# Optimization experiments

Hardware: AMD Instinct MI355X
Metric: run time of the kernel (lower is better)

Reference implementation:

```python
import jax, jax.numpy as jnp
import numpy as np

N, E, F_IN, HID, OUT, H = 50000, 500000, 128, 64, 64, 2
P_DROP = 0.2


def setup_inputs() -> dict:
    key = jax.random.key(0)
    ks = jax.random.split(key, 24)
    g = lambda k, shp: jax.random.normal(k, shp, jnp.float32) * 0.05
    inp = {
        "feat": jax.random.normal(ks[0], (N, F_IN), jnp.float32),
        "edge_src": jax.random.randint(ks[1], (E,), 0, N, jnp.int32),
        "edge_dst": jax.random.randint(ks[2], (E,), 0, N, jnp.int32),
        # feature-mask linears
        "Wmt": g(ks[3], (F_IN, F_IN)), "bmt": g(ks[4], (F_IN,)),
        "Wms": g(ks[5], (F_IN, F_IN)), "bms": g(ks[6], (F_IN,)),
        # SAGEConv layers (mean aggregator): self + neigh linear + bias
        "W1_self": g(ks[7], (F_IN, HID)), "W1_neigh": g(ks[8], (F_IN, HID)), "b1": g(ks[9], (HID,)),
        "W2_self": g(ks[10], (HID, OUT)), "W2_neigh": g(ks[11], (HID, OUT)), "b2": g(ks[12], (OUT,)),
        # GATv2Conv layers: fc_src, fc_dst, attn vector per head, bias
        "g1_Wsrc": g(ks[13], (F_IN, H * HID)), "g1_Wdst": g(ks[14], (F_IN, H * HID)),
        "g1_attn": g(ks[15], (H, HID)), "g1_bias": g(ks[16], (H * HID,)),
        "g2_Wsrc": g(ks[17], (HID, H * OUT)), "g2_Wdst": g(ks[18], (HID, H * OUT)),
        "g2_attn": g(ks[19], (H, OUT)), "g2_bias": g(ks[20], (H * OUT,)),
        # final projection
        "W3": g(ks[21], (OUT + F_IN, OUT)), "b3": g(ks[22], (OUT,)),
    }
    # deterministic (inverted) dropout masks, training=True, p=0.2
    keep = 1.0 - P_DROP
    km1, km2 = jax.random.split(ks[23])
    inp["drop_t"] = jax.random.bernoulli(km1, keep, (N, HID)).astype(jnp.float32) / keep
    inp["drop_s"] = jax.random.bernoulli(km2, keep, (N, HID)).astype(jnp.float32) / keep
    return inp


def _sage_mean(h, src, dst, W_self, W_neigh, b):
    # mean over in-neighbors, then linear (mean and linear commute)
    agg = jax.ops.segment_sum(h[src], dst, num_segments=N)          # [N,D]
    deg = jax.ops.segment_sum(jnp.ones((E,), h.dtype), dst, num_segments=N)
    h_neigh = agg / jnp.maximum(deg, 1.0)[:, None]
    return h @ W_self + h_neigh @ W_neigh + b


def _gatv2(h, src, dst, Wsrc, Wdst, attn, bias, heads, dout):
    fs = (h @ Wsrc).reshape(N, heads, dout)
    fd = (h @ Wdst).reshape(N, heads, dout)
    e = jax.nn.leaky_relu(fs[src] + fd[dst], 0.2)                   # [E,H,D]
    logits = jnp.einsum('ehd,hd->eh', e, attn)                      # [E,H]
    m = jax.ops.segment_max(logits, dst, num_segments=N)            # edge softmax per dst
    ex = jnp.exp(logits - m[dst])
    denom = jax.ops.segment_sum(ex, dst, num_segments=N)
    alpha = ex / denom[dst]                                         # [E,H]
    out = jax.ops.segment_sum(alpha[:, :, None] * fs[src], dst, num_segments=N)
    return out + bias.reshape(heads, dout)                          # [N,H,D]


def _l2norm(x):
    return x / jnp.maximum(jnp.linalg.norm(x, axis=1, keepdims=True), 1e-12)


def reference(feat, edge_src, edge_dst, Wmt, bmt, Wms, bms,
              W1_self, W1_neigh, b1, W2_self, W2_neigh, b2,
              g1_Wsrc, g1_Wdst, g1_attn, g1_bias,
              g2_Wsrc, g2_Wdst, g2_attn, g2_bias,
              W3, b3, drop_t, drop_s):
    gelu = lambda x: jax.nn.gelu(x, approximate=False)  # torch F.gelu default = exact erf
    # topology branch (SAGE)
    h_t = feat * jax.nn.sigmoid(feat @ Wmt + bmt)
    h_t = gelu(_sage_mean(h_t, edge_src, edge_dst, W1_self, W1_neigh, b1)) * drop_t
    h_t = gelu(_sage_mean(h_t, edge_src, edge_dst, W2_self, W2_neigh, b2))
    h_t = jnp.concatenate([h_t, feat], axis=1) @ W3 + b3
    h_t = _l2norm(jax.nn.leaky_relu(h_t, 0.01))
    # semantic branch (GATv2)
    h_s = feat * jax.nn.sigmoid(feat @ Wms + bms)
    h_s = gelu(_gatv2(h_s, edge_src, edge_dst, g1_Wsrc, g1_Wdst, g1_attn, g1_bias, H, HID)).mean(axis=1) * drop_s
    h_s = gelu(_gatv2(h_s, edge_src, edge_dst, g2_Wsrc, g2_Wdst, g2_attn, g2_bias, H, OUT)).mean(axis=1)
    h_s = _l2norm(h_s)
    return (h_t, h_s)
```

## Files before the change

kernel.cpp:

```cpp
#include <hip/hip_runtime.h>
#include <math.h>

constexpr int N_  = 50000;
constexpr int E_  = 500000;
constexpr int NB_ = (N_ + 255) / 256;

typedef unsigned short u16;
typedef unsigned int u32;
typedef short short8 __attribute__((ext_vector_type(8)));
typedef __bf16 bf16x8 __attribute__((ext_vector_type(8)));
typedef float f32x4 __attribute__((ext_vector_type(4)));
typedef short short4v __attribute__((ext_vector_type(4)));

#define DINL __device__ __forceinline__

DINL float gelu_f(float x) { return 0.5f * x * (1.f + erff(x * 0.70710678118654752f)); }
DINL float sigmoid_f(float x) { return 1.f / (1.f + expf(-x)); }
DINL u16 f2b(float x) {
  unsigned u = __float_as_uint(x);
  return (u16)((u + 0x7FFFu + ((u >> 16) & 1u)) >> 16);
}
DINL float b2f(u16 b) { return __uint_as_float(((unsigned)b) << 16); }

template <int CTRL>
DINL float dpp_add(float c) {
  int p = __builtin_amdgcn_update_dpp(0, __builtin_bit_cast(int, c), CTRL, 0xf, 0xf, false);
  return c + __builtin_bit_cast(float, p);
}
DINL float reduce16(float c) {
  c = dpp_add<0xB1>(c);
  c = dpp_add<0x4E>(c);
  c = dpp_add<0x141>(c);
  c = dpp_add<0x140>(c);
  return c;
}

__global__ void deg_int_kernel(const int* __restrict__ dst, int* __restrict__ deg) {
  int t = blockIdx.x * 256 + threadIdx.x;
  if (t < E_) atomicAdd(&deg[dst[t]], 1);
}

__global__ __launch_bounds__(256) void scan_local(const int* __restrict__ deg,
    int* __restrict__ rowptr, int* __restrict__ bsum) {
  __shared__ int sums[4];
  const int tid = threadIdx.x, lane = tid & 63, wid = tid >> 6;
  const int i = blockIdx.x * 256 + tid;
  int v = (i < N_) ? deg[i] : 0;
  int x = v;
#pragma unroll
  for (int o = 1; o < 64; o <<= 1) { int y = __shfl_up(x, o); if (lane >= o) x += y; }
  if (lane == 63) sums[wid] = x;
  __syncthreads();
  int woff = 0;
#pragma unroll
  for (int w = 0; w < 3; ++w) if (w < wid) woff += sums[w];
  if (i < N_) rowptr[i] = x - v + woff;
  if (tid == 255) bsum[blockIdx.x] = woff + x;
}

__global__ __launch_bounds__(256) void scan_block(const int* __restrict__ bsum,
                                                  int* __restrict__ bpre) {
  __shared__ int sums[4];
  const int tid = threadIdx.x, lane = tid & 63, wid = tid >> 6;
  int v = (tid < NB_) ? bsum[tid] : 0;
  int x = v;
#pragma unroll
  for (int o = 1; o < 64; o <<= 1) { int y = __shfl_up(x, o); if (lane >= o) x += y; }
  if (lane == 63) sums[wid] = x;
  __syncthreads();
  int woff = 0;
#pragma unroll
  for (int w = 0; w < 3; ++w) if (w < wid) woff += sums[w];
  if (tid < NB_) bpre[tid] = x - v + woff;
  if (tid == 255) bpre[NB_] = woff + x;
}

__global__ __launch_bounds__(256) void scan_add(int* __restrict__ rowptr,
                                                const int* __restrict__ bpre) {
  int i = blockIdx.x * 256 + threadIdx.x;
  if (i < N_) rowptr[i] += bpre[i >> 8];
  else if (i == N_) rowptr[N_] = bpre[NB_];
}

__global__ void csr_fill(const int* __restrict__ src, const int* __restrict__ dst,
                         const int* __restrict__ rowptr, int* __restrict__ cursor,
                         int* __restrict__ colsrc) {
  int e = blockIdx.x * 256 + threadIdx.x;
  if (e >= E_) return;
  int d = dst[e];
  int pos = rowptr[d] + atomicAdd(&cursor[d], 1);
  colsrc[pos] = src[e];
}

__global__ __launch_bounds__(256) void pack_feat(const float* __restrict__ f,
                                                 u16* __restrict__ o) {
  int t = blockIdx.x * 256 + threadIdx.x;
  float4 v = ((const float4*)f)[t];
  short4v r;
  r[0] = (short)f2b(v.x); r[1] = (short)f2b(v.y);
  r[2] = (short)f2b(v.z); r[3] = (short)f2b(v.w);
  ((short4v*)o)[t] = r;
}

__global__ __launch_bounds__(256) void pack_w(
    const float* __restrict__ Wmt, const float* __restrict__ Wms,
    const float* __restrict__ W1s, const float* __restrict__ W1n,
    const float* __restrict__ W2s, const float* __restrict__ W2n,
    const float* __restrict__ g1Ws, const float* __restrict__ g1Wd,
    const float* __restrict__ g2Ws, const float* __restrict__ g2Wd,
    const float* __restrict__ W3, u16* __restrict__ dst) {
  int e = blockIdx.x * 256 + threadIdx.x;
  const float *Wa, *Wb = nullptr;
  int K1, K2 = 0, Ca, Cb = 0, st;
  if (e < 16384)       { Wa = Wmt;  K1 = 128; Ca = 128;           st = 0; }
  else if (e < 32768)  { Wa = Wms;  K1 = 128; Ca = 128;           st = 16384; }
  else if (e < 49152)  { Wa = W1s;  Wb = W1n; K1 = 128; K2 = 128; Ca = 64;  st = 32768; }
  else if (e < 57344)  { Wa = W2s;  Wb = W2n; K1 = 64;  K2 = 64;  Ca = 64;  st = 49152; }
  else if (e < 90112)  { Wa = g1Ws; Wb = g1Wd; K1 = 128; Ca = 128; Cb = 128; st = 57344; }
  else if (e < 106496) { Wa = g2Ws; Wb = g2Wd; K1 = 64;  Ca = 128; Cb = 128; st = 90112; }
  else                 { Wa = W3;   K1 = 192; Ca = 64;            st = 106496; }
  int el = e - st;
  int Kt = K1 + K2;
  int ct = el / (Kt * 16);
  int rem = el - ct * Kt * 16;
  int ks = rem >> 9, rem2 = rem & 511, lane = rem2 >> 3, j = rem2 & 7;
  int k = ks * 32 + ((lane >> 4) << 3) + j;
  int c = ct * 16 + (lane & 15);
  float v;
  if (k < K1) v = (c < Ca) ? Wa[k * Ca + c] : Wb[k * Cb + (c - Ca)];
  else        v = Wb[(k - K1) * Ca + c];
  dst[e] = f2b(v);
}

template <int K1, int K2, int C, int EPI>
__global__ __launch_bounds__(512) void gemm_mfma(
    const u16* __restrict__ A1, const u16* __restrict__ A2,
    const u16* __restrict__ Wp, const float* __restrict__ bias,
    const float* __restrict__ bias2, const float* __restrict__ mulf,
    void* __restrict__ outv, void* __restrict__ outv2) {
  constexpr int K = K1 + K2, KS = K / 32, CT4 = C / 64;
  constexpr int NCH1 = K1 / 8, NCH2 = K2 / 8;
  __shared__ u16 alds[64 * K];
  const int tid = threadIdx.x;
  const int w = tid >> 6, l = tid & 63;
  const int cq = w >> 1, rh = w & 1;
  const int wr0 = blockIdx.x * 64;

  short8 wfrag[KS][CT4];
#pragma unroll
  for (int ks = 0; ks < KS; ++ks)
#pragma unroll
    for (int c4 = 0; c4 < CT4; ++c4)
      wfrag[ks][c4] = *(const short8*)(Wp +
          ((size_t)((cq * CT4 + c4) * KS + ks) * 64 + l) * 8);

  for (int i = tid; i < 64 * NCH1; i += 512) {
    int rr = i / NCH1, kc = i % NCH1;
    int gr = wr0 + rr; if (gr >= N_) gr = N_ - 1;
    short8 v = *(const short8*)(A1 + (long)gr * K1 + kc * 8);
    *(short8*)&alds[rr * K + ((kc ^ (rr & 7)) << 3)] = v;
  }
  if constexpr (K2 > 0) {
    for (int i = tid; i < 64 * NCH2; i += 512) {
      int rr = i / NCH2, kc = i % NCH2;
      int gr = wr0 + rr; if (gr >= N_) gr = N_ - 1;
      short8 v = *(const short8*)(A2 + (long)gr * K2 + kc * 8);
      *(short8*)&alds[rr * K + (((NCH1 + kc) ^ (rr & 7)) << 3)] = v;
    }
  }
  __syncthreads();

  f32x4 acc[2][CT4];
#pragma unroll
  for (int rr = 0; rr < 2; ++rr)
#pragma unroll
    for (int c4 = 0; c4 < CT4; ++c4) acc[rr][c4] = (f32x4){0.f, 0.f, 0.f, 0.f};

#pragma unroll
  for (int ks = 0; ks < KS; ++ks) {
#pragma unroll
    for (int rr = 0; rr < 2; ++rr) {
      const int nr = (rh * 2 + rr) * 16 + (l & 15);
      const int ch = (ks * 4 + (l >> 4)) ^ (nr & 7);
      short8 av = *(const short8*)&alds[nr * K + (ch << 3)];
      bf16x8 bf = __builtin_bit_cast(bf16x8, av);
#pragma unroll
      for (int c4 = 0; c4 < CT4; ++c4)
        acc[rr][c4] = __builtin_amdgcn_mfma_f32_16x16x32_bf16(
            __builtin_bit_cast(bf16x8, wfrag[ks][c4]), bf, acc[rr][c4], 0, 0, 0);
    }
  }

  const int colq = (l >> 4) << 2;
  if constexpr (EPI == 0) {
    u16* out = (u16*)outv;
#pragma unroll
    for (int rr = 0; rr < 2; ++rr) {
      int row = wr0 + (rh * 2 + rr) * 16 + (l & 15);
      if (row >= N_) continue;
#pragma unroll
      for (int c4 = 0; c4 < CT4; ++c4) {
        int colb = (cq * CT4 + c4) * 16 + colq;
        short4v s;
#pragma unroll
        for (int r = 0; r < 4; ++r) s[r] = (short)f2b(acc[rr][c4][r]);
        *(short4v*)(out + (long)row * C + colb) = s;
      }
    }
  } else if constexpr (EPI == 2 || EPI == 3) {
    u16* out = (u16*)outv;
    const int colb = cq * 16 + colq;
    float4 bv = *(const float4*)(bias + colb);
#pragma unroll
    for (int rr = 0; rr < 2; ++rr) {
      int row = wr0 + (rh * 2 + rr) * 16 + (l & 15);
      if (row >= N_) continue;
      float4 dv;
      if constexpr (EPI == 2) dv = *(const float4*)(mulf + (long)row * C + colb);
      short4v s;
#pragma unroll
      for (int r = 0; r < 4; ++r) {
        float g = gelu_f(acc[rr][0][r] + ((const float*)&bv)[r]);
        if constexpr (EPI == 2) g *= ((const float*)&dv)[r];
        s[r] = (short)f2b(g);
      }
      *(short4v*)(out + (long)row * C + colb) = s;
    }
  } else if constexpr (EPI == 4) {
    __shared__ float ssb[64][4];
    float* out = (float*)outv;
    const int colb = cq * 16 + colq;
    float4 bv = *(const float4*)(bias + colb);
    float xv[2][4];
#pragma unroll
    for (int rr = 0; rr < 2; ++rr) {
      float ss = 0.f;
#pragma unroll
      for (int r = 0; r < 4; ++r) {
        float x = acc[rr][0][r] + ((const float*)&bv)[r];
        x = fmaxf(x, 0.01f * x);
        xv[rr][r] = x; ss += x * x;
      }
      ss += __shfl_xor(ss, 16);
      ss += __shfl_xor(ss, 32);
      if (l < 16) ssb[(rh * 2 + rr) * 16 + l][cq] = ss;
    }
    __syncthreads();
#pragma unroll
    for (int rr = 0; rr < 2; ++rr) {
      int nl = (rh * 2 + rr) * 16 + (l & 15);
      int row = wr0 + nl;
      if (row >= N_) continue;
      float ss = ssb[nl][0] + ssb[nl][1] + ssb[nl][2] + ssb[nl][3];
      float sc = 1.f / fmaxf(sqrtf(ss), 1e-12f);
      float4 o;
#pragma unroll
      for (int r = 0; r < 4; ++r) ((float*)&o)[r] = xv[rr][r] * sc;
      *(float4*)(out + (long)row * 64 + colb) = o;
    }
  } else {
#pragma unroll
    for (int c4 = 0; c4 < CT4; ++c4) {
      const int ct = cq * CT4 + c4;
      const bool lo = ct < 8;
      u16* op = lo ? (u16*)outv : (u16*)outv2;
      const int ccb = (ct & 7) * 16 + colq;
      float4 bv = *(const float4*)((lo ? bias : bias2) + ccb);
#pragma unroll
      for (int rr = 0; rr < 2; ++rr) {
        int nl = (rh * 2 + rr) * 16 + (l & 15);
        int row = wr0 + nl;
        if (row >= N_) continue;
        int ch = (ccb >> 3) ^ (nl & 7);
        short4v fq = *(const short4v*)&alds[nl * K + (ch << 3) + (ccb & 7)];
        short4v s;
#pragma unroll
        for (int r = 0; r < 4; ++r) {
          float x = acc[rr][c4][r] + ((const float*)&bv)[r];
          float fv = b2f((u16)fq[r]);
          s[r] = (short)f2b(fv * sigmoid_f(x));
        }
        *(short4v*)(op + (long)row * 128 + ccb) = s;
      }
    }
  }
}

__global__ __launch_bounds__(256) void gather_bf128(const u16* __restrict__ h,
    const int* __restrict__ rowptr, const int* __restrict__ colsrc,
    u16* __restrict__ out) {
  int node = blockIdx.x * 4 + (threadIdx.x >> 6);
  int l = threadIdx.x & 63;
  int hl = l & 31, half = l >> 5;
  int beg = rowptr[node], end = rowptr[node + 1];
  float inv = 1.f / fmaxf((float)(end - beg), 1.f);
  float a0 = 0.f, a1 = 0.f, a2 = 0.f, a3 = 0.f;
  float b0 = 0.f, b1 = 0.f, b2 = 0.f, b3 = 0.f;
  const int off = 4 * hl;
  int j = beg;
  for (; j + 8 <= end; j += 8) {
    int sa = colsrc[j + half],     sb = colsrc[j + 2 + half];
    int sc = colsrc[j + 4 + half], sd = colsrc[j + 6 + half];
    uint2 va = *(const uint2*)(h + (size_t)sa * 128 + off);
    uint2 vb = *(const uint2*)(h + (size_t)sb * 128 + off);
    uint2 vc = *(const uint2*)(h + (size_t)sc * 128 + off);
    uint2 vd = *(const uint2*)(h + (size_t)sd * 128 + off);
    a0 += b2f((u16)(va.x & 0xffffu)) + b2f((u16)(vc.x & 0xffffu));
    a1 += b2f((u16)(va.x >> 16))     + b2f((u16)(vc.x >> 16));
    a2 += b2f((u16)(va.y & 0xffffu)) + b2f((u16)(vc.y & 0xffffu));
    a3 += b2f((u16)(va.y >> 16))     + b2f((u16)(vc.y >> 16));
    b0 += b2f((u16)(vb.x & 0xffffu)) + b2f((u16)(vd.x & 0xffffu));
    b1 += b2f((u16)(vb.x >> 16))     + b2f((u16)(vd.x >> 16));
    b2 += b2f((u16)(vb.y & 0xffffu)) + b2f((u16)(vd.y & 0xffffu));
    b3 += b2f((u16)(vb.y >> 16))     + b2f((u16)(vd.y >> 16));
  }
  for (; j < end; j += 2) {
    int idx = j + half;
    bool valid = idx < end;
    int s = colsrc[valid ? idx : end - 1];
    uint2 v = *(const uint2*)(h + (size_t)s * 128 + off);
    if (!valid) { v.x = 0; v.y = 0; }
    a0 += b2f((u16)(v.x & 0xffffu));
    a1 += b2f((u16)(v.x >> 16));
    a2 += b2f((u16)(v.y & 0xffffu));
    a3 += b2f((u16)(v.y >> 16));
  }
  a0 += b0; a1 += b1; a2 += b2; a3 += b3;
  a0 += __shfl_xor(a0, 32); a1 += __shfl_xor(a1, 32);
  a2 += __shfl_xor(a2, 32); a3 += __shfl_xor(a3, 32);
  if (l < 32) {
    short4v s;
    s[0] = (short)f2b(a0 * inv); s[1] = (short)f2b(a1 * inv);
    s[2] = (short)f2b(a2 * inv); s[3] = (short)f2b(a3 * inv);
    *(short4v*)(out + (long)node * 128 + off) = s;
  }
}

__global__ __launch_bounds__(256) void gather_bf64(const u16* __restrict__ h,
    const int* __restrict__ rowptr, const int* __restrict__ colsrc,
    u16* __restrict__ out) {
  int node = blockIdx.x * 4 + (threadIdx.x >> 6);
  int l = threadIdx.x & 63;
  int ql = l & 15, qg = l >> 4;
  int beg = rowptr[node], end = rowptr[node + 1];
  float a0 = 0.f, a1 = 0.f, a2 = 0.f, a3 = 0.f;
  float b0 = 0.f, b1 = 0.f, b2 = 0.f, b3 = 0.f;
  const int off = 4 * ql;
  int j = beg;
  for (; j + 8 <= end; j += 8) {
    int s0 = colsrc[j + qg], s1 = colsrc[j + 4 + qg];
    uint2 v0 = *(const uint2*)(h + (size_t)s0 * 64 + off);
    uint2 v1 = *(const uint2*)(h + (size_t)s1 * 64 + off);
    a0 += b2f((u16)(v0.x & 0xffffu));
    a1 += b2f((u16)(v0.x >> 16));
    a2 += b2f((u16)(v0.y & 0xffffu));
    a3 += b2f((u16)(v0.y >> 16));
    b0 += b2f((u16)(v1.x & 0xffffu));
    b1 += b2f((u16)(v1.x >> 16));
    b2 += b2f((u16)(v1.y & 0xffffu));
    b3 += b2f((u16)(v1.y >> 16));
  }
  for (; j < end; j += 4) {
    int idx = j + qg;
    bool valid = idx < end;
    int s = colsrc[valid ? idx : end - 1];
    uint2 v = *(const uint2*)(h + (size_t)s * 64 + off);
    if (!valid) { v.x = 0; v.y = 0; }
    a0 += b2f((u16)(v.x & 0xffffu));
    a1 += b2f((u16)(v.x >> 16));
    a2 += b2f((u16)(v.y & 0xffffu));
    a3 += b2f((u16)(v.y >> 16));
  }
  a0 += b0; a1 += b1; a2 += b2; a3 += b3;
  a0 += __shfl_xor(a0, 32); a1 += __shfl_xor(a1, 32);
  a2 += __shfl_xor(a2, 32); a3 += __shfl_xor(a3, 32);
  a0 += __shfl_xor(a0, 16); a1 += __shfl_xor(a1, 16);
  a2 += __shfl_xor(a2, 16); a3 += __shfl_xor(a3, 16);
  if (l < 16) {
    float inv = 1.f / fmaxf((float)(end - beg), 1.f);
    short4v s;
    s[0] = (short)f2b(a0 * inv); s[1] = (short)f2b(a1 * inv);
    s[2] = (short)f2b(a2 * inv); s[3] = (short)f2b(a3 * inv);
    *(short4v*)(out + (long)node * 64 + off) = s;
  }
}

template <bool LAYER1>
__global__ __launch_bounds__(256) void gat_fused(const u16* __restrict__ fsfd,
    const int* __restrict__ rowptr, const int* __restrict__ colsrc,
    const float* __restrict__ attn, const float* __restrict__ bias,
    const float* __restrict__ drop, void* __restrict__ outv) {
  int node = blockIdx.x * 4 + (threadIdx.x >> 6);
  int l = threadIdx.x & 63;
  int hl = l & 31, half = l >> 5;
  const int off = 4 * hl;
  float4 av = *(const float4*)(attn + off);
  uint2 fdv = *(const uint2*)(fsfd + (size_t)node * 256 + 128 + off);
  float fd0 = b2f((u16)(fdv.x & 0xffffu)), fd1 = b2f((u16)(fdv.x >> 16));
  float fd2 = b2f((u16)(fdv.y & 0xffffu)), fd3 = b2f((u16)(fdv.y >> 16));
  float d_own = 0.f, acc0 = 0.f, acc1 = 0.f, acc2 = 0.f, acc3 = 0.f;

  auto edge = [&](uint2 v, float m) {
    float f0 = b2f((u16)(v.x & 0xffffu)), f1 = b2f((u16)(v.x >> 16));
    float f2 = b2f((u16)(v.y & 0xffffu)), f3 = b2f((u16)(v.y >> 16));
    float t0 = f0 + fd0, t1 = f1 + fd1, t2 = f2 + fd2, t3 = f3 + fd3;
    t0 = fmaxf(t0, 0.2f * t0); t1 = fmaxf(t1, 0.2f * t1);
    t2 = fmaxf(t2, 0.2f * t2); t3 = fmaxf(t3, 0.2f * t3);
    float c = t0 * av.x + t1 * av.y + t2 * av.z + t3 * av.w;
    c = reduce16(c);
    float e = __expf(c) * m;
    d_own += e;
    acc0 += e * f0; acc1 += e * f1; acc2 += e * f2; acc3 += e * f3;
  };

  const int beg = rowptr[node], end = rowptr[node + 1];
  int j = beg;
  for (; j + 8 <= end; j += 8) {
    int sa = colsrc[j + half],     sb = colsrc[j + 2 + half];
    int sc = colsrc[j + 4 + half], sd = colsrc[j + 6 + half];
    uint2 va = *(const uint2*)(fsfd + (size_t)sa * 256 + off);
    uint2 vb = *(const uint2*)(fsfd + (size_t)sb * 256 + off);
    uint2 vc = *(const uint2*)(fsfd + (size_t)sc * 256 + off);
    uint2 vd = *(const uint2*)(fsfd + (size_t)sd * 256 + off);
    edge(va, 1.f); edge(vb, 1.f); edge(vc, 1.f); edge(vd, 1.f);
  }
  for (; j < end; j += 2) {
    int idx = j + half;
    bool valid = idx < end;
    int s = colsrc[valid ? idx : end - 1];
    uint2 v = *(const uint2*)(fsfd + (size_t)s * 256 + off);
    if (!valid) { v.x = 0; v.y = 0; }
    edge(v, valid ? 1.f : 0.f);
  }

  acc0 += __shfl_xor(acc0, 32); acc1 += __shfl_xor(acc1, 32);
  acc2 += __shfl_xor(acc2, 32); acc3 += __shfl_xor(acc3, 32);
  d_own += __shfl_xor(d_own, 32);

  float4 bv = *(const float4*)(bias + off);
  float inv = d_own > 0.f ? 1.f / d_own : 0.f;
  float g0 = gelu_f(bv.x + acc0 * inv);
  float g1 = gelu_f(bv.y + acc1 * inv);
  float g2 = gelu_f(bv.z + acc2 * inv);
  float g3 = gelu_f(bv.w + acc3 * inv);
  float v0 = 0.5f * (g0 + __shfl_xor(g0, 16));
  float v1 = 0.5f * (g1 + __shfl_xor(g1, 16));
  float v2 = 0.5f * (g2 + __shfl_xor(g2, 16));
  float v3 = 0.5f * (g3 + __shfl_xor(g3, 16));
  if constexpr (LAYER1) {
    if (l < 16) {
      float4 dv = *(const float4*)(drop + (long)node * 64 + 4 * l);
      short4v s;
      s[0] = (short)f2b(v0 * dv.x); s[1] = (short)f2b(v1 * dv.y);
      s[2] = (short)f2b(v2 * dv.z); s[3] = (short)f2b(v3 * dv.w);
      *(short4v*)((u16*)outv + (long)node * 64 + 4 * l) = s;
    }
  } else {
    float ss = v0 * v0 + v1 * v1 + v2 * v2 + v3 * v3;
    ss = reduce16(ss);
    float sc = 1.f / fmaxf(sqrtf(ss), 1e-12f);
    if (l < 16) {
      float4 o; o.x = v0 * sc; o.y = v1 * sc; o.z = v2 * sc; o.w = v3 * sc;
      *(float4*)((float*)outv + (long)node * 64 + 4 * l) = o;
    }
  }
}

extern "C" void kernel_launch(void* const* d_in, const int* in_sizes, int n_in,
                              void* d_out, int out_size, void* d_ws, size_t ws_size,
                              hipStream_t stream) {
  const float* feat = (const float*)d_in[0];
  const int*   esrc = (const int*)d_in[1];
  const int*   edst = (const int*)d_in[2];
  const float* Wmt = (const float*)d_in[3],  *bmt = (const float*)d_in[4];
  const float* Wms = (const float*)d_in[5],  *bms = (const float*)d_in[6];
  const float* W1s = (const float*)d_in[7],  *W1n = (const float*)d_in[8],  *b1 = (const float*)d_in[9];
  const float* W2s = (const float*)d_in[10], *W2n = (const float*)d_in[11], *b2 = (const float*)d_in[12];
  const float* g1Ws = (const float*)d_in[13], *g1Wd = (const float*)d_in[14];
  const float* g1a  = (const float*)d_in[15], *g1b  = (const float*)d_in[16];
  const float* g2Ws = (const float*)d_in[17], *g2Wd = (const float*)d_in[18];
  const float* g2a  = (const float*)d_in[19], *g2b  = (const float*)d_in[20];
  const float* W3  = (const float*)d_in[21], *b3 = (const float*)d_in[22];
  const float* dropt = (const float*)d_in[23], *drops = (const float*)d_in[24];

  float* out_t = (float*)d_out;
  float* out_s = out_t + (long)N_ * 64;

  u16* wsh = (u16*)d_ws;
  u16* featbf = wsh;
  u16* hbuf_t = wsh +  6400000;
  u16* hbuf_s = wsh + 12800000;
  u16* hn     = wsh + 19200000;
  u16* h1     = wsh + 25600000;
  u16* hn2    = wsh + 28800000;
  u16* h2     = wsh + 32000000;
  u16* hs1    = wsh + 35200000;
  u16* fsfd   = wsh + 38400000;
  u16* Wpk    = wsh + 51200000;
  int* degi   = (int*)(wsh + 51318784);
  int* cursor = degi + N_;
  int* rowptr = cursor + N_;
  int* colsrc = rowptr + N_ + 1;
  int* bsum   = colsrc + E_;
  int* bpre   = bsum + NB_;

  const u16* WpMT = Wpk;
  const u16* WpS1 = Wpk + 32768;
  const u16* WpS2 = Wpk + 49152;
  const u16* WpG1 = Wpk + 57344;
  const u16* WpG2 = Wpk + 90112;
  const u16* WpW3 = Wpk + 106496;

  constexpr int GB = (N_ + 63) / 64;

  (void)hipMemsetAsync(degi, 0, (size_t)(2 * N_) * sizeof(int), stream);
  deg_int_kernel<<<(E_ + 255) / 256, 256, 0, stream>>>(edst, degi);
  scan_local<<<NB_, 256, 0, stream>>>(degi, rowptr, bsum);
  scan_block<<<1, 256, 0, stream>>>(bsum, bpre);
  scan_add<<<(N_ + 256) / 256, 256, 0, stream>>>(rowptr, bpre);
  csr_fill<<<(E_ + 255) / 256, 256, 0, stream>>>(esrc, edst, rowptr, cursor, colsrc);
  pack_feat<<<N_ * 128 / 4 / 256, 256, 0, stream>>>(feat, featbf);
  pack_w<<<464, 256, 0, stream>>>(Wmt, Wms, W1s, W1n, W2s, W2n,
                                  g1Ws, g1Wd, g2Ws, g2Wd, W3, Wpk);

  gemm_mfma<128, 0, 256, 5><<<GB, 512, 0, stream>>>(featbf, nullptr, WpMT, bmt, bms,
                                                    nullptr, hbuf_t, hbuf_s);

  gather_bf128<<<N_ / 4, 256, 0, stream>>>(hbuf_t, rowptr, colsrc, hn);
  gemm_mfma<128, 128, 64, 2><<<GB, 512, 0, stream>>>(hbuf_t, hn, WpS1, b1, nullptr,
                                                     dropt, h1, nullptr);
  gather_bf64<<<N_ / 4, 256, 0, stream>>>(h1, rowptr, colsrc, hn2);
  gemm_mfma<64, 64, 64, 3><<<GB, 512, 0, stream>>>(h1, hn2, WpS2, b2, nullptr,
                                                   nullptr, h2, nullptr);
  gemm_mfma<64, 128, 64, 4><<<GB, 512, 0, stream>>>(h2, featbf, WpW3, b3, nullptr,
                                                    nullptr, out_t, nullptr);

  gemm_mfma<128, 0, 256, 0><<<GB, 512, 0, stream>>>(hbuf_s, nullptr, WpG1, nullptr, nullptr,
                                                    nullptr, fsfd, nullptr);
  gat_fused<true><<<N_ / 4, 256, 0, stream>>>(fsfd, rowptr, colsrc, g1a, g1b, drops, hs1);
  gemm_mfma<64, 0, 256, 0><<<GB, 512, 0, stream>>>(hs1, nullptr, WpG2, nullptr, nullptr,
                                                   nullptr, fsfd, nullptr);
  gat_fused<false><<<N_ / 4, 256, 0, stream>>>(fsfd, rowptr, colsrc, g2a, g2b, nullptr, out_s);
}
```

Measured before the change: 268.9 us.

## Project before aggregating in SAGE layers, fusing bias, gelu and dropout into gather

```diff
diff --git a/kernel.cpp b/kernel.cpp
--- a/kernel.cpp
+++ b/kernel.cpp
@@ -114,8 +114,8 @@
   int K1, K2 = 0, Ca, Cb = 0, st;
   if (e < 16384)       { Wa = Wmt;  K1 = 128; Ca = 128;           st = 0; }
   else if (e < 32768)  { Wa = Wms;  K1 = 128; Ca = 128;           st = 16384; }
-  else if (e < 49152)  { Wa = W1s;  Wb = W1n; K1 = 128; K2 = 128; Ca = 64;  st = 32768; }
-  else if (e < 57344)  { Wa = W2s;  Wb = W2n; K1 = 64;  K2 = 64;  Ca = 64;  st = 49152; }
+  else if (e < 49152)  { Wa = W1s;  Wb = W1n; K1 = 128; Ca = 64; Cb = 64; st = 32768; }
+  else if (e < 57344)  { Wa = W2s;  Wb = W2n; K1 = 64;  Ca = 64; Cb = 64; st = 49152; }
   else if (e < 90112)  { Wa = g1Ws; Wb = g1Wd; K1 = 128; Ca = 128; Cb = 128; st = 57344; }
   else if (e < 106496) { Wa = g2Ws; Wb = g2Wd; K1 = 64;  Ca = 128; Cb = 128; st = 90112; }
   else                 { Wa = W3;   K1 = 192; Ca = 64;            st = 106496; }
@@ -207,25 +207,6 @@
         *(short4v*)(out + (long)row * C + colb) = s;
       }
     }
-  } else if constexpr (EPI == 2 || EPI == 3) {
-    u16* out = (u16*)outv;
-    const int colb = cq * 16 + colq;
-    float4 bv = *(const float4*)(bias + colb);
-#pragma unroll
-    for (int rr = 0; rr < 2; ++rr) {
-      int row = wr0 + (rh * 2 + rr) * 16 + (l & 15);
-      if (row >= N_) continue;
-      float4 dv;
-      if constexpr (EPI == 2) dv = *(const float4*)(mulf + (long)row * C + colb);
-      short4v s;
-#pragma unroll
-      for (int r = 0; r < 4; ++r) {
-        float g = gelu_f(acc[rr][0][r] + ((const float*)&bv)[r]);
-        if constexpr (EPI == 2) g *= ((const float*)&dv)[r];
-        s[r] = (short)f2b(g);
-      }
-      *(short4v*)(out + (long)row * C + colb) = s;
-    }
   } else if constexpr (EPI == 4) {
     __shared__ float ssb[64][4];
     float* out = (float*)outv;
@@ -286,71 +267,23 @@
   }
 }
 
-__global__ __launch_bounds__(256) void gather_bf128(const u16* __restrict__ h,
+template <bool DROP>
+__global__ __launch_bounds__(256) void gather_sage(const u16* __restrict__ qp,
     const int* __restrict__ rowptr, const int* __restrict__ colsrc,
-    u16* __restrict__ out) {
-  int node = blockIdx.x * 4 + (threadIdx.x >> 6);
-  int l = threadIdx.x & 63;
-  int hl = l & 31, half = l >> 5;
-  int beg = rowptr[node], end = rowptr[node + 1];
-  float inv = 1.f / fmaxf((float)(end - beg), 1.f);
-  float a0 = 0.f, a1 = 0.f, a2 = 0.f, a3 = 0.f;
-  float b0 = 0.f, b1 = 0.f, b2 = 0.f, b3 = 0.f;
-  const int off = 4 * hl;
-  int j = beg;
-  for (; j + 8 <= end; j += 8) {
-    int sa = colsrc[j + half],     sb = colsrc[j + 2 + half];
-    int sc = colsrc[j + 4 + half], sd = colsrc[j + 6 + half];
-    uint2 va = *(const uint2*)(h + (size_t)sa * 128 + off);
-    uint2 vb = *(const uint2*)(h + (size_t)sb * 128 + off);
-    uint2 vc = *(const uint2*)(h + (size_t)sc * 128 + off);
-    uint2 vd = *(const uint2*)(h + (size_t)sd * 128 + off);
-    a0 += b2f((u16)(va.x & 0xffffu)) + b2f((u16)(vc.x & 0xffffu));
-    a1 += b2f((u16)(va.x >> 16))     + b2f((u16)(vc.x >> 16));
-    a2 += b2f((u16)(va.y & 0xffffu)) + b2f((u16)(vc.y & 0xffffu));
-    a3 += b2f((u16)(va.y >> 16))     + b2f((u16)(vc.y >> 16));
-    b0 += b2f((u16)(vb.x & 0xffffu)) + b2f((u16)(vd.x & 0xffffu));
-    b1 += b2f((u16)(vb.x >> 16))     + b2f((u16)(vd.x >> 16));
-    b2 += b2f((u16)(vb.y & 0xffffu)) + b2f((u16)(vd.y & 0xffffu));
-    b3 += b2f((u16)(vb.y >> 16))     + b2f((u16)(vd.y >> 16));
-  }
-  for (; j < end; j += 2) {
-    int idx = j + half;
-    bool valid = idx < end;
-    int s = colsrc[valid ? idx : end - 1];
-    uint2 v = *(const uint2*)(h + (size_t)s * 128 + off);
-    if (!valid) { v.x = 0; v.y = 0; }
-    a0 += b2f((u16)(v.x & 0xffffu));
-    a1 += b2f((u16)(v.x >> 16));
-    a2 += b2f((u16)(v.y & 0xffffu));
-    a3 += b2f((u16)(v.y >> 16));
-  }
-  a0 += b0; a1 += b1; a2 += b2; a3 += b3;
-  a0 += __shfl_xor(a0, 32); a1 += __shfl_xor(a1, 32);
-  a2 += __shfl_xor(a2, 32); a3 += __shfl_xor(a3, 32);
-  if (l < 32) {
-    short4v s;
-    s[0] = (short)f2b(a0 * inv); s[1] = (short)f2b(a1 * inv);
-    s[2] = (short)f2b(a2 * inv); s[3] = (short)f2b(a3 * inv);
-    *(short4v*)(out + (long)node * 128 + off) = s;
-  }
-}
-
-__global__ __launch_bounds__(256) void gather_bf64(const u16* __restrict__ h,
-    const int* __restrict__ rowptr, const int* __restrict__ colsrc,
+    const float* __restrict__ bias, const float* __restrict__ drop,
     u16* __restrict__ out) {
   int node = blockIdx.x * 4 + (threadIdx.x >> 6);
   int l = threadIdx.x & 63;
   int ql = l & 15, qg = l >> 4;
   int beg = rowptr[node], end = rowptr[node + 1];
+  const int off = 4 * ql;
   float a0 = 0.f, a1 = 0.f, a2 = 0.f, a3 = 0.f;
   float b0 = 0.f, b1 = 0.f, b2 = 0.f, b3 = 0.f;
-  const int off = 4 * ql;
   int j = beg;
   for (; j + 8 <= end; j += 8) {
     int s0 = colsrc[j + qg], s1 = colsrc[j + 4 + qg];
-    uint2 v0 = *(const uint2*)(h + (size_t)s0 * 64 + off);
-    uint2 v1 = *(const uint2*)(h + (size_t)s1 * 64 + off);
+    uint2 v0 = *(const uint2*)(qp + (size_t)s0 * 128 + 64 + off);
+    uint2 v1 = *(const uint2*)(qp + (size_t)s1 * 128 + 64 + off);
     a0 += b2f((u16)(v0.x & 0xffffu));
     a1 += b2f((u16)(v0.x >> 16));
     a2 += b2f((u16)(v0.y & 0xffffu));
@@ -364,7 +297,7 @@
     int idx = j + qg;
     bool valid = idx < end;
     int s = colsrc[valid ? idx : end - 1];
-    uint2 v = *(const uint2*)(h + (size_t)s * 64 + off);
+    uint2 v = *(const uint2*)(qp + (size_t)s * 128 + 64 + off);
     if (!valid) { v.x = 0; v.y = 0; }
     a0 += b2f((u16)(v.x & 0xffffu));
     a1 += b2f((u16)(v.x >> 16));
@@ -378,9 +311,19 @@
   a2 += __shfl_xor(a2, 16); a3 += __shfl_xor(a3, 16);
   if (l < 16) {
     float inv = 1.f / fmaxf((float)(end - beg), 1.f);
+    uint2 qv = *(const uint2*)(qp + (size_t)node * 128 + off);
+    float4 bv = *(const float4*)(bias + off);
+    float g0 = gelu_f(b2f((u16)(qv.x & 0xffffu)) + a0 * inv + bv.x);
+    float g1 = gelu_f(b2f((u16)(qv.x >> 16))     + a1 * inv + bv.y);
+    float g2 = gelu_f(b2f((u16)(qv.y & 0xffffu)) + a2 * inv + bv.z);
+    float g3 = gelu_f(b2f((u16)(qv.y >> 16))     + a3 * inv + bv.w);
+    if constexpr (DROP) {
+      float4 dv = *(const float4*)(drop + (long)node * 64 + off);
+      g0 *= dv.x; g1 *= dv.y; g2 *= dv.z; g3 *= dv.w;
+    }
     short4v s;
-    s[0] = (short)f2b(a0 * inv); s[1] = (short)f2b(a1 * inv);
-    s[2] = (short)f2b(a2 * inv); s[3] = (short)f2b(a3 * inv);
+    s[0] = (short)f2b(g0); s[1] = (short)f2b(g1);
+    s[2] = (short)f2b(g2); s[3] = (short)f2b(g3);
     *(short4v*)(out + (long)node * 64 + off) = s;
   }
 }
@@ -490,14 +433,14 @@
   u16* featbf = wsh;
   u16* hbuf_t = wsh +  6400000;
   u16* hbuf_s = wsh + 12800000;
-  u16* hn     = wsh + 19200000;
+  u16* qp1    = wsh + 19200000;
   u16* h1     = wsh + 25600000;
-  u16* hn2    = wsh + 28800000;
-  u16* h2     = wsh + 32000000;
-  u16* hs1    = wsh + 35200000;
-  u16* fsfd   = wsh + 38400000;
-  u16* Wpk    = wsh + 51200000;
-  int* degi   = (int*)(wsh + 51318784);
+  u16* qp2    = wsh + 28800000;
+  u16* h2     = wsh + 35200000;
+  u16* hs1    = wsh + 38400000;
+  u16* fsfd   = wsh + 41600000;
+  u16* Wpk    = wsh + 54400000;
+  int* degi   = (int*)(wsh + 54518784);
   int* cursor = degi + N_;
   int* rowptr = cursor + N_;
   int* colsrc = rowptr + N_ + 1;
@@ -526,12 +469,12 @@
   gemm_mfma<128, 0, 256, 5><<<GB, 512, 0, stream>>>(featbf, nullptr, WpMT, bmt, bms,
                                                     nullptr, hbuf_t, hbuf_s);
 
-  gather_bf128<<<N_ / 4, 256, 0, stream>>>(hbuf_t, rowptr, colsrc, hn);
-  gemm_mfma<128, 128, 64, 2><<<GB, 512, 0, stream>>>(hbuf_t, hn, WpS1, b1, nullptr,
-                                                     dropt, h1, nullptr);
-  gather_bf64<<<N_ / 4, 256, 0, stream>>>(h1, rowptr, colsrc, hn2);
-  gemm_mfma<64, 64, 64, 3><<<GB, 512, 0, stream>>>(h1, hn2, WpS2, b2, nullptr,
-                                                   nullptr, h2, nullptr);
+  gemm_mfma<128, 0, 128, 0><<<GB, 512, 0, stream>>>(hbuf_t, nullptr, WpS1, nullptr, nullptr,
+                                                    nullptr, qp1, nullptr);
+  gather_sage<true><<<N_ / 4, 256, 0, stream>>>(qp1, rowptr, colsrc, b1, dropt, h1);
+  gemm_mfma<64, 0, 128, 0><<<GB, 512, 0, stream>>>(h1, nullptr, WpS2, nullptr, nullptr,
+                                                   nullptr, qp2, nullptr);
+  gather_sage<false><<<N_ / 4, 256, 0, stream>>>(qp2, rowptr, colsrc, b2, nullptr, h2);
   gemm_mfma<64, 128, 64, 4><<<GB, 512, 0, stream>>>(h2, featbf, WpW3, b3, nullptr,
                                                     nullptr, out_t, nullptr);
 
```

New measurement: 272.3 us. Within noise of the previous version (+1.3%).
